# Performance work log

Measured on AMD Instinct MI355X. Metric: run time of the kernel, lower is better.

Reference implementation:

```python
import jax, jax.numpy as jnp
import numpy as np

Ts = 1.0  # simulation time step from netParams['simulation']


def _alpha_filter(x, tau):
    # Causal SRM-alpha PSP filter along time (leading axis):
    #   y[t] = Ts * sum_{k>=0} (k*Ts/tau) * exp(1 - k*Ts/tau) * x[t-k]
    # Implemented as an exact 2-state linear recurrence (IIR form of the alpha kernel).
    d = jnp.float32(np.exp(-Ts / tau))
    c = jnp.float32(np.e * Ts / tau * Ts)  # kernel scale * Ts integration factor

    def step(carry, xt):
        P, Q = carry           # P[t] = sum x[j] d^{t-j}; Q[t] = sum x[j] (t-j) d^{t-j}
        Q = d * (Q + P)
        P = d * P + xt
        return (P, Q), c * Q

    z = jnp.zeros_like(x[0])
    _, y = jax.lax.scan(step, (z, z), x)
    return y


def _make_spike(theta, tauRho, scaleRho):
    # SLAYER spike function: Heaviside forward, surrogate-gradient backward
    pdf_scale = scaleRho / (tauRho * theta)
    pdf_tc = tauRho * theta

    @jax.custom_vjp
    def spike(u):
        return (u >= theta).astype(u.dtype)

    def fwd(u):
        return spike(u), u

    def bwd(u, g):
        return (g * pdf_scale * jnp.exp(-jnp.abs(u - theta) / pdf_tc),)

    spike.defvjp(fwd, bwd)
    return spike


def _lif_spike(u_in, theta, tauRef, scaleRef, tauRho, scaleRho):
    # Sequential leaky integrate-and-fire with alpha refractory kernel:
    #   u[t] = u_in[t] - scaleRef*theta * sum_{j<t} s[j] * (dt/tauRef)*exp(1-dt/tauRef), dt=(t-j)*Ts
    # Refractory alpha kernel realized by the same 2-state recurrence, fed by emitted spikes.
    d = jnp.float32(np.exp(-Ts / tauRef))
    ref_gain = jnp.float32(scaleRef * theta * np.e * Ts / tauRef)
    spike = _make_spike(theta, tauRho, scaleRho)

    def step(carry, ut):
        P, Q = carry
        Q = d * (Q + P)            # refractory kernel value (zero at lag 0)
        s = spike(ut - ref_gain * Q)
        P = d * P + s              # inject this step's spikes
        return (P, Q), s

    z = jnp.zeros_like(u_in[0])
    _, s = jax.lax.scan(step, (z, z), u_in)
    return s


def _conv2d_t(x, w, pad):
    # x: [T, N, C, H, W] -> same spatial conv applied at every timestep (slayer conv = Conv3d with kT=1)
    T, N, C, H, W = x.shape
    y = jax.lax.conv_general_dilated(
        x.reshape(T * N, C, H, W), w,
        window_strides=(1, 1), padding=[(pad, pad), (pad, pad)],
        dimension_numbers=('NCHW', 'OIHW', 'NCHW'))
    return y.reshape(T, N, -1, H, W)


def _forward(spikeInput, conv1_w, conv2_w):
    # spikeInput: [N, C, H, W, T] -> scan over leading time axis
    x = jnp.transpose(spikeInput, (4, 0, 1, 2, 3))
    psp1 = _alpha_filter(x, tau=1.0)                                        # slayer1.psp (tauSr=1)
    s1 = _lif_spike(_conv2d_t(psp1, conv1_w, 2),
                    theta=30.0, tauRef=1.0, scaleRef=1.0, tauRho=1.0, scaleRho=10.0)
    psp2 = _alpha_filter(s1, tau=2.0)                                       # slayer2.psp (tauSr=2)
    s2 = _lif_spike(_conv2d_t(psp2, conv2_w, 1),
                    theta=50.0, tauRef=2.0, scaleRef=1.0, tauRho=1.0, scaleRho=10.0)
    return jnp.transpose(s2, (1, 2, 3, 4, 0))  # back to [N, C, H, W, T]


def setup_inputs() -> dict:
    key = jax.random.key(0)
    k1, k2, k3 = jax.random.split(key, 3)
    spikeInput = (jax.random.uniform(k1, (2, 8, 128, 128, 64)) < 0.1).astype(jnp.float32)
    # slayer conv uses weightScale-amplified weights, bias-free; scale so thresholds are reachable
    conv1_w = jax.random.normal(k2, (8, 8, 5, 5), jnp.float32) * 2.0
    conv2_w = jax.random.normal(k3, (8, 8, 3, 3), jnp.float32) * 2.0
    return {"spikeInput": spikeInput, "conv1_w": conv1_w, "conv2_w": conv2_w}


def reference(spikeInput, conv1_w, conv2_w):
    return _forward(spikeInput, conv1_w, conv2_w)
```

## Files before the change

kernel.cpp:

```cpp
#include <hip/hip_runtime.h>

#define TN 64
#define NB 2
#define CH 8
#define HH 128
#define WW 128
#define HW (HH*WW)
#define CHW (CH*HW)
#define NCHW (NB*CHW)

__global__ __launch_bounds__(256) void k_psp1(const float* __restrict__ x,
                                              float* __restrict__ psp1) {
    int e = blockIdx.x * blockDim.x + threadIdx.x;
    if (e >= NCHW) return;
    const float d1 = 0.36787944117144233f;
    const float c1 = 2.7182818284590452f;
    float P = 0.f, Q = 0.f;
    const float4* xe = reinterpret_cast<const float4*>(x + (size_t)e * TN);
    #pragma unroll
    for (int t4 = 0; t4 < TN / 4; ++t4) {
        float4 xv = xe[t4];
        float xs[4] = {xv.x, xv.y, xv.z, xv.w};
        #pragma unroll
        for (int j = 0; j < 4; ++j) {
            Q = d1 * (Q + P);
            P = d1 * P + xs[j];
            psp1[(size_t)(t4 * 4 + j) * NCHW + e] = c1 * Q;
        }
    }
}

__global__ __launch_bounds__(256, 4) void k_conv1(const float* __restrict__ in,
                                                  const float* __restrict__ w1,
                                                  float* __restrict__ outp) {
    __shared__ __align__(16) float tile[2][12][136];
    const int img = blockIdx.y;
    const int h0 = blockIdx.x * 8;
    const int tid = threadIdx.x;
    const int yi = tid >> 5;
    const int x0 = (tid & 31) * 4;
    const float* base = in + (size_t)img * CHW;

    int goff[7];
    #pragma unroll
    for (int k = 0; k < 7; ++k) {
        int idx = tid + (k << 8);
        int r = idx / 136;
        int c = idx - r * 136;
        int gh = h0 + r - 2, gw = c - 2;
        bool ok = (idx < 1632) && (gh >= 0) && (gh < HH) && (gw >= 0) && (gw < WW);
        goff[k] = ok ? (gh * WW + gw) : -1;
    }

    float va[7];
    #pragma unroll
    for (int k = 0; k < 7; ++k) {
        int g = goff[k];
        int gc = g < 0 ? 0 : g;
        float t0 = base[gc];
        va[k] = g < 0 ? 0.f : t0;
    }

    float acc[CH][4];
    #pragma unroll
    for (int co = 0; co < CH; ++co)
        #pragma unroll
        for (int xo = 0; xo < 4; ++xo) acc[co][xo] = 0.f;

    for (int ci = 0; ci < CH; ++ci) {
        float* dst = &tile[ci & 1][0][0];
        #pragma unroll
        for (int k = 0; k < 7; ++k) {
            int idx = tid + (k << 8);
            if (k < 6 || idx < 1632) dst[idx] = va[k];
        }
        if (ci < 7) {
            const float* nb = base + (size_t)(ci + 1) * HW;
            #pragma unroll
            for (int k = 0; k < 7; ++k) {
                int g = goff[k];
                int gc = g < 0 ? 0 : g;
                float t0 = nb[gc];
                va[k] = g < 0 ? 0.f : t0;
            }
        }
        __syncthreads();

        const float* chp = &tile[ci & 1][0][0];
        #pragma unroll
        for (int ky = 0; ky < 5; ++ky) {
            const float4* rp =
                reinterpret_cast<const float4*>(chp + (yi + ky) * 136 + x0);
            float4 A = rp[0], B = rp[1];
            float f[8] = {A.x, A.y, A.z, A.w, B.x, B.y, B.z, B.w};
            #pragma unroll
            for (int co = 0; co < CH; ++co) {
                const float* wp = w1 + (co * CH + ci) * 25 + ky * 5;
                #pragma unroll
                for (int kx = 0; kx < 5; ++kx) {
                    float wv = wp[kx];
                    #pragma unroll
                    for (int xo = 0; xo < 4; ++xo)
                        acc[co][xo] = fmaf(wv, f[kx + xo], acc[co][xo]);
                }
            }
        }
    }

    float* ob = outp + (size_t)img * CHW + (h0 + yi) * WW + x0;
    #pragma unroll
    for (int co = 0; co < CH; ++co)
        *reinterpret_cast<float4*>(ob + co * HW) =
            make_float4(acc[co][0], acc[co][1], acc[co][2], acc[co][3]);
}

__global__ __launch_bounds__(256) void k_lif1_psp2(const float* __restrict__ u1,
                                                   float* __restrict__ psp2) {
    int e2 = blockIdx.x * blockDim.x + threadIdx.x;
    if (e2 >= NCHW / 2) return;
    const float dr = 0.36787944117144233f;
    const float rg = 81.54845485377136f;
    const float th = 30.f;
    const float d2 = 0.60653065971263342f;
    const float c2 = 1.35914091422952262f;
    float Pr0 = 0.f, Qr0 = 0.f, P20 = 0.f, Q20 = 0.f;
    float Pr1 = 0.f, Qr1 = 0.f, P21 = 0.f, Q21 = 0.f;
    const float2* ue = reinterpret_cast<const float2*>(u1);
    float2* oe = reinterpret_cast<float2*>(psp2);
    #pragma unroll 8
    for (int t = 0; t < TN; ++t) {
        float2 uv = ue[(size_t)t * (NCHW / 2) + e2];
        Qr0 = dr * (Qr0 + Pr0);
        float s0 = (uv.x - rg * Qr0 >= th) ? 1.0f : 0.0f;
        Pr0 = dr * Pr0 + s0;
        Q20 = d2 * (Q20 + P20);
        P20 = d2 * P20 + s0;
        Qr1 = dr * (Qr1 + Pr1);
        float s1 = (uv.y - rg * Qr1 >= th) ? 1.0f : 0.0f;
        Pr1 = dr * Pr1 + s1;
        Q21 = d2 * (Q21 + P21);
        P21 = d2 * P21 + s1;
        oe[(size_t)t * (NCHW / 2) + e2] = make_float2(c2 * Q20, c2 * Q21);
    }
}

__global__ __launch_bounds__(256, 4) void k_conv2(const float* __restrict__ in,
                                                  const float* __restrict__ w2,
                                                  float* __restrict__ outp) {
    __shared__ __align__(16) float tile[2][10][136];
    const int img = blockIdx.y;
    const int h0 = blockIdx.x * 8;
    const int tid = threadIdx.x;
    const int yi = tid >> 5;
    const int x0 = (tid & 31) * 4;
    const float* base = in + (size_t)img * CHW;

    int goff[6];
    #pragma unroll
    for (int k = 0; k < 6; ++k) {
        int idx = tid + (k << 8);
        int r = idx / 136;
        int c = idx - r * 136;
        int gh = h0 + r - 1, gw = c - 1;
        bool ok = (idx < 1360) && (gh >= 0) && (gh < HH) && (gw >= 0) && (gw < WW);
        goff[k] = ok ? (gh * WW + gw) : -1;
    }

    float va[6];
    #pragma unroll
    for (int k = 0; k < 6; ++k) {
        int g = goff[k];
        int gc = g < 0 ? 0 : g;
        float t0 = base[gc];
        va[k] = g < 0 ? 0.f : t0;
    }

    float acc[CH][4];
    #pragma unroll
    for (int co = 0; co < CH; ++co)
        #pragma unroll
        for (int xo = 0; xo < 4; ++xo) acc[co][xo] = 0.f;

    for (int ci = 0; ci < CH; ++ci) {
        float* dst = &tile[ci & 1][0][0];
        #pragma unroll
        for (int k = 0; k < 6; ++k) {
            int idx = tid + (k << 8);
            if (k < 5 || idx < 1360) dst[idx] = va[k];
        }
        if (ci < 7) {
            const float* nb = base + (size_t)(ci + 1) * HW;
            #pragma unroll
            for (int k = 0; k < 6; ++k) {
                int g = goff[k];
                int gc = g < 0 ? 0 : g;
                float t0 = nb[gc];
                va[k] = g < 0 ? 0.f : t0;
            }
        }
        __syncthreads();

        const float* chp = &tile[ci & 1][0][0];
        #pragma unroll
        for (int ky = 0; ky < 3; ++ky) {
            const float4* rp =
                reinterpret_cast<const float4*>(chp + (yi + ky) * 136 + x0);
            float4 A = rp[0], B = rp[1];
            float f[8] = {A.x, A.y, A.z, A.w, B.x, B.y, B.z, B.w};
            #pragma unroll
            for (int co = 0; co < CH; ++co) {
                const float* wp = w2 + (co * CH + ci) * 9 + ky * 3;
                #pragma unroll
                for (int kx = 0; kx < 3; ++kx) {
                    float wv = wp[kx];
                    #pragma unroll
                    for (int xo = 0; xo < 4; ++xo)
                        acc[co][xo] = fmaf(wv, f[kx + xo], acc[co][xo]);
                }
            }
        }
    }

    float* ob = outp + (size_t)img * CHW + (h0 + yi) * WW + x0;
    #pragma unroll
    for (int co = 0; co < CH; ++co)
        *reinterpret_cast<float4*>(ob + co * HW) =
            make_float4(acc[co][0], acc[co][1], acc[co][2], acc[co][3]);
}

__global__ __launch_bounds__(256) void k_lif2(const float* __restrict__ u2,
                                              float* __restrict__ outp) {
    int e = blockIdx.x * blockDim.x + threadIdx.x;
    if (e >= NCHW) return;
    const float dr = 0.60653065971263342f;
    const float rg = 67.95704571147613f;
    const float th = 50.f;
    float Pr = 0.f, Qr = 0.f;
    float sv[TN];
    #pragma unroll
    for (int t = 0; t < TN; ++t) {
        Qr = dr * (Qr + Pr);
        float u = u2[(size_t)t * NCHW + e];
        float s = (u - rg * Qr >= th) ? 1.0f : 0.0f;
        Pr = dr * Pr + s;
        sv[t] = s;
    }
    float4* o = reinterpret_cast<float4*>(outp + (size_t)e * TN);
    #pragma unroll
    for (int i = 0; i < TN / 4; ++i)
        o[i] = make_float4(sv[4 * i], sv[4 * i + 1], sv[4 * i + 2], sv[4 * i + 3]);
}

extern "C" void kernel_launch(void* const* d_in, const int* in_sizes, int n_in,
                              void* d_out, int out_size, void* d_ws, size_t ws_size,
                              hipStream_t stream) {
    const float* x  = (const float*)d_in[0];
    const float* w1 = (const float*)d_in[1];
    const float* w2 = (const float*)d_in[2];
    float* out = (float*)d_out;

    float* bufA = (float*)d_ws;
    float* bufB = bufA + (size_t)TN * NCHW;

    dim3 blk(256);
    dim3 grd_pt(NCHW / 256);
    dim3 grd_pt2(NCHW / 512);
    dim3 grd_cv(16, TN * NB);

    k_psp1<<<grd_pt, blk, 0, stream>>>(x, bufA);
    k_conv1<<<grd_cv, blk, 0, stream>>>(bufA, w1, bufB);
    k_lif1_psp2<<<grd_pt2, blk, 0, stream>>>(bufB, bufA);
    k_conv2<<<grd_cv, blk, 0, stream>>>(bufA, w2, bufB);
    k_lif2<<<grd_pt, blk, 0, stream>>>(bufB, out);
}
```

Baseline: 194.5 us.

## Commute alpha filters past convolutions so convs read binary spikes as bytes

Because the alpha PSP filter is linear in time and the convolution is linear in space, the filter is moved after each convolution and folded into the LIF kernels. The convolutions then read binary spike tensors stored as uint8 instead of float PSP tensors, which cuts intermediate memory traffic about fourfold. The input is transposed to time-major uint8 through LDS, and spikes from layer one are written as bytes. The reordering changes floating-point summation order, so spikes near threshold may flip.

```diff
diff --git a/kernel.cpp b/kernel.cpp
--- a/kernel.cpp
+++ b/kernel.cpp
@@ -9,28 +9,36 @@
 #define CHW (CH*HW)
 #define NCHW (NB*CHW)
 
-__global__ __launch_bounds__(256) void k_psp1(const float* __restrict__ x,
-                                              float* __restrict__ psp1) {
-    int e = blockIdx.x * blockDim.x + threadIdx.x;
-    if (e >= NCHW) return;
-    const float d1 = 0.36787944117144233f;
-    const float c1 = 2.7182818284590452f;
-    float P = 0.f, Q = 0.f;
-    const float4* xe = reinterpret_cast<const float4*>(x + (size_t)e * TN);
-    #pragma unroll
-    for (int t4 = 0; t4 < TN / 4; ++t4) {
-        float4 xv = xe[t4];
-        float xs[4] = {xv.x, xv.y, xv.z, xv.w};
-        #pragma unroll
-        for (int j = 0; j < 4; ++j) {
-            Q = d1 * (Q + P);
-            P = d1 * P + xs[j];
-            psp1[(size_t)(t4 * 4 + j) * NCHW + e] = c1 * Q;
-        }
-    }
-}
-
-__global__ __launch_bounds__(256, 4) void k_conv1(const float* __restrict__ in,
+
+__global__ __launch_bounds__(256) void k_tr(const float* __restrict__ x,
+                                            unsigned char* __restrict__ xT) {
+    __shared__ unsigned char lds[256 * 68];
+    const int tid = threadIdx.x;
+    const size_t e0 = (size_t)blockIdx.x * 256;
+    const float4* xb = reinterpret_cast<const float4*>(x + (e0 + tid) * TN);
+    unsigned int* lds32 = reinterpret_cast<unsigned int*>(lds);
+    #pragma unroll
+    for (int k = 0; k < 16; ++k) {
+        float4 v = xb[k];
+        unsigned int p = ((unsigned)v.x) | (((unsigned)v.y) << 8) |
+                         (((unsigned)v.z) << 16) | (((unsigned)v.w) << 24);
+        lds32[tid * 17 + k] = p;
+    }
+    __syncthreads();
+    const int lane = tid & 63, w = tid >> 6;
+    #pragma unroll
+    for (int k = 0; k < 16; ++k) {
+        int t = w * 16 + k;
+        unsigned int b0 = lds[(4 * lane + 0) * 68 + t];
+        unsigned int b1 = lds[(4 * lane + 1) * 68 + t];
+        unsigned int b2 = lds[(4 * lane + 2) * 68 + t];
+        unsigned int b3 = lds[(4 * lane + 3) * 68 + t];
+        unsigned int p = b0 | (b1 << 8) | (b2 << 16) | (b3 << 24);
+        *reinterpret_cast<unsigned int*>(xT + (size_t)t * NCHW + e0 + 4 * lane) = p;
+    }
+}
+
+__global__ __launch_bounds__(256, 4) void k_conv1(const unsigned char* __restrict__ in,
                                                   const float* __restrict__ w1,
                                                   float* __restrict__ outp) {
     __shared__ __align__(16) float tile[2][12][136];
@@ -39,7 +47,7 @@
     const int tid = threadIdx.x;
     const int yi = tid >> 5;
     const int x0 = (tid & 31) * 4;
-    const float* base = in + (size_t)img * CHW;
+    const unsigned char* base = in + (size_t)img * CHW;
 
     int goff[7];
     #pragma unroll
@@ -57,7 +65,7 @@
     for (int k = 0; k < 7; ++k) {
         int g = goff[k];
         int gc = g < 0 ? 0 : g;
-        float t0 = base[gc];
+        float t0 = (float)base[gc];
         va[k] = g < 0 ? 0.f : t0;
     }
 
@@ -75,12 +83,12 @@
             if (k < 6 || idx < 1632) dst[idx] = va[k];
         }
         if (ci < 7) {
-            const float* nb = base + (size_t)(ci + 1) * HW;
+            const unsigned char* nb = base + (size_t)(ci + 1) * HW;
             #pragma unroll
             for (int k = 0; k < 7; ++k) {
                 int g = goff[k];
                 int gc = g < 0 ? 0 : g;
-                float t0 = nb[gc];
+                float t0 = (float)nb[gc];
                 va[k] = g < 0 ? 0.f : t0;
             }
         }
@@ -114,37 +122,35 @@
             make_float4(acc[co][0], acc[co][1], acc[co][2], acc[co][3]);
 }
 
-__global__ __launch_bounds__(256) void k_lif1_psp2(const float* __restrict__ u1,
-                                                   float* __restrict__ psp2) {
+__global__ __launch_bounds__(256) void k_alif1(const float* __restrict__ v1,
+                                               unsigned char* __restrict__ s1) {
     int e2 = blockIdx.x * blockDim.x + threadIdx.x;
     if (e2 >= NCHW / 2) return;
+    const float d1 = 0.36787944117144233f;
+    const float c1 = 2.7182818284590452f;
     const float dr = 0.36787944117144233f;
     const float rg = 81.54845485377136f;
     const float th = 30.f;
-    const float d2 = 0.60653065971263342f;
-    const float c2 = 1.35914091422952262f;
-    float Pr0 = 0.f, Qr0 = 0.f, P20 = 0.f, Q20 = 0.f;
-    float Pr1 = 0.f, Qr1 = 0.f, P21 = 0.f, Q21 = 0.f;
-    const float2* ue = reinterpret_cast<const float2*>(u1);
-    float2* oe = reinterpret_cast<float2*>(psp2);
+    float P0 = 0.f, Q0 = 0.f, Pr0 = 0.f, Qr0 = 0.f;
+    float P1 = 0.f, Q1 = 0.f, Pr1 = 0.f, Qr1 = 0.f;
+    const float2* ve = reinterpret_cast<const float2*>(v1);
     #pragma unroll 8
     for (int t = 0; t < TN; ++t) {
-        float2 uv = ue[(size_t)t * (NCHW / 2) + e2];
+        float2 v = ve[(size_t)t * (NCHW / 2) + e2];
+        Q0 = d1 * (Q0 + P0); P0 = d1 * P0 + v.x;
         Qr0 = dr * (Qr0 + Pr0);
-        float s0 = (uv.x - rg * Qr0 >= th) ? 1.0f : 0.0f;
+        float s0 = (c1 * Q0 - rg * Qr0 >= th) ? 1.0f : 0.0f;
         Pr0 = dr * Pr0 + s0;
-        Q20 = d2 * (Q20 + P20);
-        P20 = d2 * P20 + s0;
+        Q1 = d1 * (Q1 + P1); P1 = d1 * P1 + v.y;
         Qr1 = dr * (Qr1 + Pr1);
-        float s1 = (uv.y - rg * Qr1 >= th) ? 1.0f : 0.0f;
-        Pr1 = dr * Pr1 + s1;
-        Q21 = d2 * (Q21 + P21);
-        P21 = d2 * P21 + s1;
-        oe[(size_t)t * (NCHW / 2) + e2] = make_float2(c2 * Q20, c2 * Q21);
-    }
-}
-
-__global__ __launch_bounds__(256, 4) void k_conv2(const float* __restrict__ in,
+        float s1v = (c1 * Q1 - rg * Qr1 >= th) ? 1.0f : 0.0f;
+        Pr1 = dr * Pr1 + s1v;
+        uchar2 o; o.x = (unsigned char)s0; o.y = (unsigned char)s1v;
+        *reinterpret_cast<uchar2*>(s1 + (size_t)t * NCHW + 2 * e2) = o;
+    }
+}
+
+__global__ __launch_bounds__(256, 4) void k_conv2(const unsigned char* __restrict__ in,
                                                   const float* __restrict__ w2,
                                                   float* __restrict__ outp) {
     __shared__ __align__(16) float tile[2][10][136];
@@ -153,7 +159,7 @@
     const int tid = threadIdx.x;
     const int yi = tid >> 5;
     const int x0 = (tid & 31) * 4;
-    const float* base = in + (size_t)img * CHW;
+    const unsigned char* base = in + (size_t)img * CHW;
 
     int goff[6];
     #pragma unroll
@@ -171,7 +177,7 @@
     for (int k = 0; k < 6; ++k) {
         int g = goff[k];
         int gc = g < 0 ? 0 : g;
-        float t0 = base[gc];
+        float t0 = (float)base[gc];
         va[k] = g < 0 ? 0.f : t0;
     }
 
@@ -189,12 +195,12 @@
             if (k < 5 || idx < 1360) dst[idx] = va[k];
         }
         if (ci < 7) {
-            const float* nb = base + (size_t)(ci + 1) * HW;
+            const unsigned char* nb = base + (size_t)(ci + 1) * HW;
             #pragma unroll
             for (int k = 0; k < 6; ++k) {
                 int g = goff[k];
                 int gc = g < 0 ? 0 : g;
-                float t0 = nb[gc];
+                float t0 = (float)nb[gc];
                 va[k] = g < 0 ? 0.f : t0;
             }
         }
@@ -228,20 +234,23 @@
             make_float4(acc[co][0], acc[co][1], acc[co][2], acc[co][3]);
 }
 
-__global__ __launch_bounds__(256) void k_lif2(const float* __restrict__ u2,
-                                              float* __restrict__ outp) {
+__global__ __launch_bounds__(256) void k_alif2(const float* __restrict__ v2,
+                                               float* __restrict__ outp) {
     int e = blockIdx.x * blockDim.x + threadIdx.x;
     if (e >= NCHW) return;
+    const float d2 = 0.60653065971263342f;
+    const float c2 = 1.35914091422952262f;
     const float dr = 0.60653065971263342f;
     const float rg = 67.95704571147613f;
     const float th = 50.f;
-    float Pr = 0.f, Qr = 0.f;
+    float P = 0.f, Q = 0.f, Pr = 0.f, Qr = 0.f;
     float sv[TN];
     #pragma unroll
     for (int t = 0; t < TN; ++t) {
+        Q = d2 * (Q + P);
+        P = d2 * P + v2[(size_t)t * NCHW + e];
         Qr = dr * (Qr + Pr);
-        float u = u2[(size_t)t * NCHW + e];
-        float s = (u - rg * Qr >= th) ? 1.0f : 0.0f;
+        float s = (c2 * Q - rg * Qr >= th) ? 1.0f : 0.0f;
         Pr = dr * Pr + s;
         sv[t] = s;
     }
@@ -259,17 +268,18 @@
     const float* w2 = (const float*)d_in[2];
     float* out = (float*)d_out;
 
-    float* bufA = (float*)d_ws;
-    float* bufB = bufA + (size_t)TN * NCHW;
+    float* vbuf = (float*)d_ws;
+    unsigned char* xT = (unsigned char*)d_ws + (size_t)TN * NCHW * 4;
+    unsigned char* s1 = xT + (size_t)TN * NCHW;
 
     dim3 blk(256);
     dim3 grd_pt(NCHW / 256);
     dim3 grd_pt2(NCHW / 512);
     dim3 grd_cv(16, TN * NB);
 
-    k_psp1<<<grd_pt, blk, 0, stream>>>(x, bufA);
-    k_conv1<<<grd_cv, blk, 0, stream>>>(bufA, w1, bufB);
-    k_lif1_psp2<<<grd_pt2, blk, 0, stream>>>(bufB, bufA);
-    k_conv2<<<grd_cv, blk, 0, stream>>>(bufA, w2, bufB);
-    k_lif2<<<grd_pt, blk, 0, stream>>>(bufB, out);
-}
+    k_tr<<<grd_pt, blk, 0, stream>>>(x, xT);
+    k_conv1<<<grd_cv, blk, 0, stream>>>(xT, w1, vbuf);
+    k_alif1<<<grd_pt2, blk, 0, stream>>>(vbuf, s1);
+    k_conv2<<<grd_cv, blk, 0, stream>>>(s1, w2, vbuf);
+    k_alif2<<<grd_pt, blk, 0, stream>>>(vbuf, out);
+}
```

Measured after the change: 180.8 us. 7.0% less time.
